# Optimization experiments

Measured on AMD Instinct MI355X. Metric: run time of the kernel, lower is better.

The kernel has to match this reference:

```python
import jax, jax.numpy as jnp
import numpy as np

B, S, E, H = 8, 2048, 1024, 64

def setup_inputs() -> dict:
    key = jax.random.key(0)
    k1, k2, k3, k4 = jax.random.split(key, 4)
    scale = 0.02
    return {
        "x": jax.random.normal(k1, (B, S, E), dtype=jnp.float32),
        "Wq": jax.random.normal(k2, (E, H), dtype=jnp.float32) * scale,
        "Wk": jax.random.normal(k3, (E, H), dtype=jnp.float32) * scale,
        "Wv": jax.random.normal(k4, (E, H), dtype=jnp.float32) * scale,
    }

def reference(x, Wq, Wk, Wv):
    # x: [B, S, E]; projections to [B, S, H]
    q = jnp.einsum("bse,eh->bsh", x, Wq)
    k = jnp.einsum("bse,eh->bsh", x, Wk)
    v = jnp.einsum("bse,eh->bsh", x, Wv)
    head_size = Wq.shape[1]
    # NOTE: original divides by head_size (not sqrt(head_size))
    scores = jnp.einsum("bqh,bkh->bqk", q, k) / head_size  # [B, S, S]
    seq = q.shape[1]
    causal = jnp.tril(jnp.ones((seq, seq), dtype=bool))
    scores = jnp.where(causal, scores, -jnp.inf)
    attn = jax.nn.softmax(scores, axis=-1)
    # dropout p=0.0 (eval) -> identity
    return jnp.einsum("bqk,bkh->bqh", attn, v)
```

## Files before the change

kernel.cpp:

```cpp
#include <hip/hip_runtime.h>


typedef __bf16 bf16;
typedef bf16 bf16x8 __attribute__((ext_vector_type(8)));
typedef bf16 bf16x4 __attribute__((ext_vector_type(4)));
typedef float v4f __attribute__((ext_vector_type(4)));

#define MFMA_BF16 __builtin_amdgcn_mfma_f32_16x16x32_bf16

constexpr int SEQ = 2048, EDIM = 1024, HDIM = 64;
constexpr float SCALE_L2E = 1.4426950408889634f / 64.0f;

#define AS1 __attribute__((address_space(1)))
#define AS3 __attribute__((address_space(3)))
static __device__ __forceinline__ void gload_lds16(const void* g, void* l) {
  __builtin_amdgcn_global_load_lds((const AS1 unsigned int*)g,
                                   (AS3 unsigned int*)l, 16, 0, 0);
}

__global__ __launch_bounds__(256) void prep_w_kernel(
    const float* __restrict__ Wq, const float* __restrict__ Wk,
    const float* __restrict__ Wv, bf16* __restrict__ Wt) {
  int mat = blockIdx.x >> 5, kseg = blockIdx.x & 31;
  const float* src = mat == 0 ? Wq : (mat == 1 ? Wk : Wv);
  int n = threadIdx.x & 63;
  int k0 = kseg * 32 + (threadIdx.x >> 6) * 8;
  bf16x8 v;
#pragma unroll
  for (int j = 0; j < 8; ++j)
    v[j] = (bf16)src[(k0 + j) * 64 + n];
  *reinterpret_cast<bf16x8*>(Wt + (size_t)(mat * 64 + n) * EDIM + k0) = v;
}

__global__ __launch_bounds__(256, 3) void proj_kernel(
    const float* __restrict__ x, const bf16* __restrict__ Wt,
    bf16* __restrict__ qw, bf16* __restrict__ kw, bf16* __restrict__ vT) {
  __shared__ __align__(16) bf16 Bs[2][192][64];
  __shared__ __align__(16) bf16 Ash[32][64];

  const int t = threadIdx.x;
  const int m0 = blockIdx.x * 32;
  const int wv = t >> 6, lane = t & 63, quad = lane >> 4, l16 = lane & 15;
  const int arow = t >> 3;
  const int aslot = t & 7;

  v4f acc[2][3] = {};
  float4 aR0, aR1;

  auto loadA = [&](int kk) {
    const float* p = x + (size_t)(m0 + arow) * EDIM + kk * 64 + aslot * 8;
    aR0 = *reinterpret_cast<const float4*>(p);
    aR1 = *reinterpret_cast<const float4*>(p + 4);
  };
  auto writeA = [&]() {
    bf16x8 h = {(bf16)aR0.x, (bf16)aR0.y, (bf16)aR0.z, (bf16)aR0.w,
                (bf16)aR1.x, (bf16)aR1.y, (bf16)aR1.z, (bf16)aR1.w};
    *reinterpret_cast<bf16x8*>((char*)&Ash[0][0] + arow * 128 +
                               ((aslot ^ (arow & 7)) * 16)) = h;
  };
  auto issueB = [&](int kk, int buf) {
#pragma unroll
    for (int p = 0; p < 6; ++p) {
      int q = p * 64 + lane;
      int r = 48 * wv + (q >> 3), s = q & 7;
      const bf16* src = Wt + (size_t)r * EDIM + kk * 64 + (s ^ (r & 7)) * 8;
      bf16* dst = &Bs[buf][48 * wv + 8 * p][0];
      gload_lds16(src, dst);
    }
  };

  loadA(0);
  issueB(0, 0);
  asm volatile("s_waitcnt vmcnt(6)" ::: "memory");
  __builtin_amdgcn_sched_barrier(0);
  writeA();
  asm volatile("s_waitcnt lgkmcnt(0)" ::: "memory");
  __builtin_amdgcn_s_barrier();

#pragma unroll 1
  for (int kk = 0; kk < 16; ++kk) {
    const int buf = kk & 1;
    if (kk < 15) {
      loadA(kk + 1);
      issueB(kk + 1, buf ^ 1);
      asm volatile("s_waitcnt vmcnt(8)" ::: "memory");
    } else {
      asm volatile("s_waitcnt vmcnt(0)" ::: "memory");
    }
    __builtin_amdgcn_sched_barrier(0);

    const char* asb = (const char*)&Ash[0][0];
    const char* bsb = (const char*)&Bs[buf][0][0];
    bf16x8 af[2][2];
#pragma unroll
    for (int mi = 0; mi < 2; ++mi)
#pragma unroll
      for (int ks = 0; ks < 2; ++ks) {
        int row = 16 * mi + l16;
        int off = ((4 * ks + quad) ^ (row & 7)) * 16;
        af[mi][ks] = *reinterpret_cast<const bf16x8*>(asb + row * 128 + off);
      }
#pragma unroll
    for (int ks = 0; ks < 2; ++ks) {
      bf16x8 bfr[3];
#pragma unroll
      for (int ni = 0; ni < 3; ++ni) {
        int R = 48 * wv + 16 * ni + l16;
        int off = (ks * 64 + quad * 16) ^ ((R & 7) << 4);
        bfr[ni] = *reinterpret_cast<const bf16x8*>(bsb + R * 128 + off);
      }
#pragma unroll
      for (int mi = 0; mi < 2; ++mi)
#pragma unroll
        for (int ni = 0; ni < 3; ++ni)
          acc[mi][ni] = MFMA_BF16(af[mi][ks], bfr[ni], acc[mi][ni], 0, 0, 0);
    }

    if (kk < 15) {
      asm volatile("s_waitcnt lgkmcnt(0)" ::: "memory");
      __builtin_amdgcn_sched_barrier(0);
      __builtin_amdgcn_s_barrier();
      asm volatile("s_waitcnt vmcnt(6)" ::: "memory");
      __builtin_amdgcn_sched_barrier(0);
      writeA();
      asm volatile("s_waitcnt lgkmcnt(0)" ::: "memory");
      __builtin_amdgcn_sched_barrier(0);
      __builtin_amdgcn_s_barrier();
    }
  }

#pragma unroll
  for (int mi = 0; mi < 2; ++mi) {
    const int token0 = m0 + 16 * mi + 4 * quad;
#pragma unroll
    for (int ni = 0; ni < 3; ++ni) {
      int n = 48 * wv + 16 * ni + l16;
      if (n < 64) {
#pragma unroll
        for (int r = 0; r < 4; ++r)
          qw[(size_t)(token0 + r) * HDIM + n] = (bf16)acc[mi][ni][r];
      } else if (n < 128) {
#pragma unroll
        for (int r = 0; r < 4; ++r)
          kw[(size_t)(token0 + r) * HDIM + (n - 64)] = (bf16)acc[mi][ni][r];
      } else {
        int b = token0 >> 11, s0 = token0 & 2047;
        bf16x4 pk = {(bf16)acc[mi][ni][0], (bf16)acc[mi][ni][1],
                     (bf16)acc[mi][ni][2], (bf16)acc[mi][ni][3]};
        *reinterpret_cast<bf16x4*>(
            vT + ((size_t)(b * 64 + (n - 128))) * SEQ + s0) = pk;
      }
    }
  }
}

__global__ __launch_bounds__(512) void attn_kernel(
    const bf16* __restrict__ qw, const bf16* __restrict__ kw,
    const bf16* __restrict__ vT, float* __restrict__ out) {
  const int batch = blockIdx.x & 7;
  const int pi = blockIdx.x >> 3;
  const int w = threadIdx.x >> 6;
  const int lane = threadIdx.x & 63;
  const int quad = lane >> 4, l16 = lane & 15;

  __shared__ __align__(16) bf16 p_lds[8][2][32][68];
  __shared__ __align__(16) float o_lds[8][32][68];
  __shared__ float l_lds[8][32];

  const bf16* qB = qw + (size_t)batch * SEQ * HDIM;
  const bf16* kB = kw + (size_t)batch * SEQ * HDIM;
  const bf16* vB = vT + (size_t)batch * HDIM * SEQ;

  for (int sp = 0; sp < 2; ++sp) {
    const int j = sp ? (63 - pi) : pi;
    const int q0 = 32 * j;
    const int T64 = (j + 2) >> 1;
    const int nw = (T64 > w) ? (((T64 - 1 - w) >> 3) + 1) : 0;

    bf16x8 aq[2][2];
#pragma unroll
    for (int mi = 0; mi < 2; ++mi)
#pragma unroll
      for (int kf = 0; kf < 2; ++kf)
        aq[mi][kf] = *reinterpret_cast<const bf16x8*>(
            qB + (size_t)(q0 + 16 * mi + l16) * HDIM + 32 * kf + 8 * quad);

    v4f accO[2][4] = {};
    float l_part[2][4] = {{0.f, 0.f, 0.f, 0.f}, {0.f, 0.f, 0.f, 0.f}};
    bf16x8 kfr[4][2];

    auto loadK = [&](int jt) {
#pragma unroll
      for (int nt = 0; nt < 4; ++nt)
#pragma unroll
        for (int kf = 0; kf < 2; ++kf)
          kfr[nt][kf] = *reinterpret_cast<const bf16x8*>(
              kB + (size_t)(64 * jt + 16 * nt + l16) * HDIM + 32 * kf +
              8 * quad);
    };
    auto qk_exp_stage = [&](int jt, int slot) {
      v4f s[2][4] = {};
#pragma unroll
      for (int mi = 0; mi < 2; ++mi)
#pragma unroll
        for (int nt = 0; nt < 4; ++nt) {
          s[mi][nt] = MFMA_BF16(aq[mi][0], kfr[nt][0], s[mi][nt], 0, 0, 0);
          s[mi][nt] = MFMA_BF16(aq[mi][1], kfr[nt][1], s[mi][nt], 0, 0, 0);
        }
      const bool last = (jt == T64 - 1);
#pragma unroll
      for (int mi = 0; mi < 2; ++mi)
#pragma unroll
        for (int nt = 0; nt < 4; ++nt)
#pragma unroll
          for (int r = 0; r < 4; ++r) {
            float p = __builtin_amdgcn_exp2f(s[mi][nt][r] * SCALE_L2E);
            if (last &&
                (64 * jt + 16 * nt + l16 > q0 + 16 * mi + 4 * quad + r))
              p = 0.f;
            l_part[mi][r] += p;
            p_lds[w][slot][16 * mi + 4 * quad + r][16 * nt + l16] = (bf16)p;
          }
    };

    if (nw > 0) {
      loadK(w);
      qk_exp_stage(w, 0);
    }
    for (int i = 0; i < nw; ++i) {
      const int jt = w + 8 * i;
      const int k0 = 64 * jt;
      if (i + 1 < nw) loadK(jt + 8);
      bf16x8 vfr[4][2];
#pragma unroll
      for (int nt = 0; nt < 4; ++nt)
#pragma unroll
        for (int kc = 0; kc < 2; ++kc)
          vfr[nt][kc] = *reinterpret_cast<const bf16x8*>(
              vB + (size_t)(16 * nt + l16) * SEQ + k0 + 32 * kc + 8 * quad);
      asm volatile("s_waitcnt lgkmcnt(0)" ::: "memory");
      bf16x8 pa[2][2];
#pragma unroll
      for (int mi = 0; mi < 2; ++mi)
#pragma unroll
        for (int kc = 0; kc < 2; ++kc)
          pa[mi][kc] = *reinterpret_cast<const bf16x8*>(
              &p_lds[w][i & 1][16 * mi + l16][32 * kc + 8 * quad]);
      if (i + 1 < nw) qk_exp_stage(jt + 8, (i + 1) & 1);
#pragma unroll
      for (int mi = 0; mi < 2; ++mi)
#pragma unroll
        for (int nt = 0; nt < 4; ++nt) {
          accO[mi][nt] = MFMA_BF16(pa[mi][0], vfr[nt][0], accO[mi][nt], 0, 0, 0);
          accO[mi][nt] = MFMA_BF16(pa[mi][1], vfr[nt][1], accO[mi][nt], 0, 0, 0);
        }
    }

#pragma unroll
    for (int mi = 0; mi < 2; ++mi)
#pragma unroll
      for (int r = 0; r < 4; ++r) {
        float s = l_part[mi][r];
        s += __shfl_xor(s, 1, 16);
        s += __shfl_xor(s, 2, 16);
        s += __shfl_xor(s, 4, 16);
        s += __shfl_xor(s, 8, 16);
        l_part[mi][r] = s;
      }

    __syncthreads();
#pragma unroll
    for (int mi = 0; mi < 2; ++mi)
#pragma unroll
      for (int nt = 0; nt < 4; ++nt)
#pragma unroll
        for (int r = 0; r < 4; ++r)
          o_lds[w][16 * mi + 4 * quad + r][16 * nt + l16] = accO[mi][nt][r];
    if (l16 == 0) {
#pragma unroll
      for (int mi = 0; mi < 2; ++mi)
#pragma unroll
        for (int r = 0; r < 4; ++r)
          l_lds[w][16 * mi + 4 * quad + r] = l_part[mi][r];
    }
    __syncthreads();

    {
      const int col = threadIdx.x & 63;
      const int r0 = (threadIdx.x >> 6) * 4;
#pragma unroll
      for (int k = 0; k < 4; ++k) {
        const int row = r0 + k;
        float lt = 0.f, s = 0.f;
#pragma unroll
        for (int c = 0; c < 8; ++c) {
          lt += l_lds[c][row];
          s += o_lds[c][row][col];
        }
        out[((size_t)batch * SEQ + q0 + row) * HDIM + col] = s / lt;
      }
    }
  }
}

extern "C" void kernel_launch(void* const* d_in, const int* in_sizes, int n_in,
                              void* d_out, int out_size, void* d_ws,
                              size_t ws_size, hipStream_t stream) {
  const float* x = (const float*)d_in[0];
  const float* Wq = (const float*)d_in[1];
  const float* Wk = (const float*)d_in[2];
  const float* Wv = (const float*)d_in[3];

  char* ws = (char*)d_ws;
  bf16* Wt = (bf16*)(ws);
  bf16* qw = (bf16*)(ws + 0x60000);
  bf16* kw = (bf16*)(ws + 0x260000);
  bf16* vT = (bf16*)(ws + 0x460000);

  prep_w_kernel<<<96, 256, 0, stream>>>(Wq, Wk, Wv, Wt);
  proj_kernel<<<512, 256, 0, stream>>>(x, Wt, qw, kw, vT);
  attn_kernel<<<256, 512, 0, stream>>>(qw, kw, vT, (float*)d_out);
}
```

Measured before the change: 138.3 us.

## Alias attention LDS buffers and split paired query tiles into separate blocks

Overlays the P staging buffer and the O reduction buffer in one shared allocation, halving LDS use per block so two blocks can be resident per CU. The grid doubles and each block now handles a single query tile instead of a balanced pair of short and long tiles. A launch-bounds occupancy hint is added. This trades the per-block causal load balancing for higher occupancy and latency hiding, and risks register pressure from the tighter bound.

```diff
diff --git a/kernel.cpp b/kernel.cpp
--- a/kernel.cpp
+++ b/kernel.cpp
@@ -154,151 +154,152 @@
   }
 }
 
-__global__ __launch_bounds__(512) void attn_kernel(
+__global__ __launch_bounds__(512, 4) void attn_kernel(
     const bf16* __restrict__ qw, const bf16* __restrict__ kw,
     const bf16* __restrict__ vT, float* __restrict__ out) {
-  const int batch = blockIdx.x & 7;
-  const int pi = blockIdx.x >> 3;
+  const int bid = blockIdx.x;
+  const int batch = bid & 7;
+  const int s = (bid & 255) >> 3;
+  const int j = (bid >= 256) ? (63 - s) : s;
   const int w = threadIdx.x >> 6;
   const int lane = threadIdx.x & 63;
   const int quad = lane >> 4, l16 = lane & 15;
 
-  __shared__ __align__(16) bf16 p_lds[8][2][32][68];
-  __shared__ __align__(16) float o_lds[8][32][68];
-  __shared__ float l_lds[8][32];
+  __shared__ __align__(16) char smem[70656];
+  typedef bf16 PT[2][32][68];
+  typedef float OT[32][68];
+  PT* p_lds = reinterpret_cast<PT*>(smem);
+  OT* o_lds = reinterpret_cast<OT*>(smem);
+  float(*l_lds)[32] = reinterpret_cast<float(*)[32]>(smem + 69632);
 
   const bf16* qB = qw + (size_t)batch * SEQ * HDIM;
   const bf16* kB = kw + (size_t)batch * SEQ * HDIM;
   const bf16* vB = vT + (size_t)batch * HDIM * SEQ;
 
-  for (int sp = 0; sp < 2; ++sp) {
-    const int j = sp ? (63 - pi) : pi;
-    const int q0 = 32 * j;
-    const int T64 = (j + 2) >> 1;
-    const int nw = (T64 > w) ? (((T64 - 1 - w) >> 3) + 1) : 0;
-
-    bf16x8 aq[2][2];
-#pragma unroll
-    for (int mi = 0; mi < 2; ++mi)
+  const int q0 = 32 * j;
+  const int T64 = (j + 2) >> 1;
+  const int nw = (T64 > w) ? (((T64 - 1 - w) >> 3) + 1) : 0;
+
+  bf16x8 aq[2][2];
+#pragma unroll
+  for (int mi = 0; mi < 2; ++mi)
+#pragma unroll
+    for (int kf = 0; kf < 2; ++kf)
+      aq[mi][kf] = *reinterpret_cast<const bf16x8*>(
+          qB + (size_t)(q0 + 16 * mi + l16) * HDIM + 32 * kf + 8 * quad);
+
+  v4f accO[2][4] = {};
+  float l_part[2][4] = {{0.f, 0.f, 0.f, 0.f}, {0.f, 0.f, 0.f, 0.f}};
+  bf16x8 kfr[4][2];
+
+  auto loadK = [&](int jt) {
+#pragma unroll
+    for (int nt = 0; nt < 4; ++nt)
 #pragma unroll
       for (int kf = 0; kf < 2; ++kf)
-        aq[mi][kf] = *reinterpret_cast<const bf16x8*>(
-            qB + (size_t)(q0 + 16 * mi + l16) * HDIM + 32 * kf + 8 * quad);
-
-    v4f accO[2][4] = {};
-    float l_part[2][4] = {{0.f, 0.f, 0.f, 0.f}, {0.f, 0.f, 0.f, 0.f}};
-    bf16x8 kfr[4][2];
-
-    auto loadK = [&](int jt) {
+        kfr[nt][kf] = *reinterpret_cast<const bf16x8*>(
+            kB + (size_t)(64 * jt + 16 * nt + l16) * HDIM + 32 * kf +
+            8 * quad);
+  };
+  auto qk_exp_stage = [&](int jt, int slot) {
+    v4f sc[2][4] = {};
+#pragma unroll
+    for (int mi = 0; mi < 2; ++mi)
+#pragma unroll
+      for (int nt = 0; nt < 4; ++nt) {
+        sc[mi][nt] = MFMA_BF16(aq[mi][0], kfr[nt][0], sc[mi][nt], 0, 0, 0);
+        sc[mi][nt] = MFMA_BF16(aq[mi][1], kfr[nt][1], sc[mi][nt], 0, 0, 0);
+      }
+    const bool last = (jt == T64 - 1);
+#pragma unroll
+    for (int mi = 0; mi < 2; ++mi)
 #pragma unroll
       for (int nt = 0; nt < 4; ++nt)
 #pragma unroll
-        for (int kf = 0; kf < 2; ++kf)
-          kfr[nt][kf] = *reinterpret_cast<const bf16x8*>(
-              kB + (size_t)(64 * jt + 16 * nt + l16) * HDIM + 32 * kf +
-              8 * quad);
-    };
-    auto qk_exp_stage = [&](int jt, int slot) {
-      v4f s[2][4] = {};
-#pragma unroll
-      for (int mi = 0; mi < 2; ++mi)
-#pragma unroll
-        for (int nt = 0; nt < 4; ++nt) {
-          s[mi][nt] = MFMA_BF16(aq[mi][0], kfr[nt][0], s[mi][nt], 0, 0, 0);
-          s[mi][nt] = MFMA_BF16(aq[mi][1], kfr[nt][1], s[mi][nt], 0, 0, 0);
+        for (int r = 0; r < 4; ++r) {
+          float p = __builtin_amdgcn_exp2f(sc[mi][nt][r] * SCALE_L2E);
+          if (last && (64 * jt + 16 * nt + l16 > q0 + 16 * mi + 4 * quad + r))
+            p = 0.f;
+          l_part[mi][r] += p;
+          p_lds[w][slot][16 * mi + 4 * quad + r][16 * nt + l16] = (bf16)p;
         }
-      const bool last = (jt == T64 - 1);
-#pragma unroll
-      for (int mi = 0; mi < 2; ++mi)
-#pragma unroll
-        for (int nt = 0; nt < 4; ++nt)
-#pragma unroll
-          for (int r = 0; r < 4; ++r) {
-            float p = __builtin_amdgcn_exp2f(s[mi][nt][r] * SCALE_L2E);
-            if (last &&
-                (64 * jt + 16 * nt + l16 > q0 + 16 * mi + 4 * quad + r))
-              p = 0.f;
-            l_part[mi][r] += p;
-            p_lds[w][slot][16 * mi + 4 * quad + r][16 * nt + l16] = (bf16)p;
-          }
-    };
-
-    if (nw > 0) {
-      loadK(w);
-      qk_exp_stage(w, 0);
-    }
-    for (int i = 0; i < nw; ++i) {
-      const int jt = w + 8 * i;
-      const int k0 = 64 * jt;
-      if (i + 1 < nw) loadK(jt + 8);
-      bf16x8 vfr[4][2];
-#pragma unroll
-      for (int nt = 0; nt < 4; ++nt)
-#pragma unroll
-        for (int kc = 0; kc < 2; ++kc)
-          vfr[nt][kc] = *reinterpret_cast<const bf16x8*>(
-              vB + (size_t)(16 * nt + l16) * SEQ + k0 + 32 * kc + 8 * quad);
-      asm volatile("s_waitcnt lgkmcnt(0)" ::: "memory");
-      bf16x8 pa[2][2];
-#pragma unroll
-      for (int mi = 0; mi < 2; ++mi)
-#pragma unroll
-        for (int kc = 0; kc < 2; ++kc)
-          pa[mi][kc] = *reinterpret_cast<const bf16x8*>(
-              &p_lds[w][i & 1][16 * mi + l16][32 * kc + 8 * quad]);
-      if (i + 1 < nw) qk_exp_stage(jt + 8, (i + 1) & 1);
-#pragma unroll
-      for (int mi = 0; mi < 2; ++mi)
-#pragma unroll
-        for (int nt = 0; nt < 4; ++nt) {
-          accO[mi][nt] = MFMA_BF16(pa[mi][0], vfr[nt][0], accO[mi][nt], 0, 0, 0);
-          accO[mi][nt] = MFMA_BF16(pa[mi][1], vfr[nt][1], accO[mi][nt], 0, 0, 0);
-        }
-    }
-
-#pragma unroll
-    for (int mi = 0; mi < 2; ++mi)
-#pragma unroll
-      for (int r = 0; r < 4; ++r) {
-        float s = l_part[mi][r];
-        s += __shfl_xor(s, 1, 16);
-        s += __shfl_xor(s, 2, 16);
-        s += __shfl_xor(s, 4, 16);
-        s += __shfl_xor(s, 8, 16);
-        l_part[mi][r] = s;
-      }
-
-    __syncthreads();
-#pragma unroll
-    for (int mi = 0; mi < 2; ++mi)
-#pragma unroll
-      for (int nt = 0; nt < 4; ++nt)
-#pragma unroll
-        for (int r = 0; r < 4; ++r)
-          o_lds[w][16 * mi + 4 * quad + r][16 * nt + l16] = accO[mi][nt][r];
-    if (l16 == 0) {
-#pragma unroll
-      for (int mi = 0; mi < 2; ++mi)
-#pragma unroll
-        for (int r = 0; r < 4; ++r)
-          l_lds[w][16 * mi + 4 * quad + r] = l_part[mi][r];
-    }
-    __syncthreads();
-
-    {
-      const int col = threadIdx.x & 63;
-      const int r0 = (threadIdx.x >> 6) * 4;
-#pragma unroll
-      for (int k = 0; k < 4; ++k) {
-        const int row = r0 + k;
-        float lt = 0.f, s = 0.f;
-#pragma unroll
-        for (int c = 0; c < 8; ++c) {
-          lt += l_lds[c][row];
-          s += o_lds[c][row][col];
-        }
-        out[((size_t)batch * SEQ + q0 + row) * HDIM + col] = s / lt;
-      }
+  };
+
+  if (nw > 0) {
+    loadK(w);
+    qk_exp_stage(w, 0);
+  }
+  for (int i = 0; i < nw; ++i) {
+    const int jt = w + 8 * i;
+    const int k0 = 64 * jt;
+    if (i + 1 < nw) loadK(jt + 8);
+    bf16x8 vfr[4][2];
+#pragma unroll
+    for (int nt = 0; nt < 4; ++nt)
+#pragma unroll
+      for (int kc = 0; kc < 2; ++kc)
+        vfr[nt][kc] = *reinterpret_cast<const bf16x8*>(
+            vB + (size_t)(16 * nt + l16) * SEQ + k0 + 32 * kc + 8 * quad);
+    asm volatile("s_waitcnt lgkmcnt(0)" ::: "memory");
+    bf16x8 pa[2][2];
+#pragma unroll
+    for (int mi = 0; mi < 2; ++mi)
+#pragma unroll
+      for (int kc = 0; kc < 2; ++kc)
+        pa[mi][kc] = *reinterpret_cast<const bf16x8*>(
+            &p_lds[w][i & 1][16 * mi + l16][32 * kc + 8 * quad]);
+    if (i + 1 < nw) qk_exp_stage(jt + 8, (i + 1) & 1);
+#pragma unroll
+    for (int mi = 0; mi < 2; ++mi)
+#pragma unroll
+      for (int nt = 0; nt < 4; ++nt) {
+        accO[mi][nt] = MFMA_BF16(pa[mi][0], vfr[nt][0], accO[mi][nt], 0, 0, 0);
+        accO[mi][nt] = MFMA_BF16(pa[mi][1], vfr[nt][1], accO[mi][nt], 0, 0, 0);
+      }
+  }
+
+#pragma unroll
+  for (int mi = 0; mi < 2; ++mi)
+#pragma unroll
+    for (int r = 0; r < 4; ++r) {
+      float sv = l_part[mi][r];
+      sv += __shfl_xor(sv, 1, 16);
+      sv += __shfl_xor(sv, 2, 16);
+      sv += __shfl_xor(sv, 4, 16);
+      sv += __shfl_xor(sv, 8, 16);
+      l_part[mi][r] = sv;
+    }
+
+  __syncthreads();
+#pragma unroll
+  for (int mi = 0; mi < 2; ++mi)
+#pragma unroll
+    for (int nt = 0; nt < 4; ++nt)
+#pragma unroll
+      for (int r = 0; r < 4; ++r)
+        o_lds[w][16 * mi + 4 * quad + r][16 * nt + l16] = accO[mi][nt][r];
+  if (l16 == 0) {
+#pragma unroll
+    for (int mi = 0; mi < 2; ++mi)
+#pragma unroll
+      for (int r = 0; r < 4; ++r)
+        l_lds[w][16 * mi + 4 * quad + r] = l_part[mi][r];
+  }
+  __syncthreads();
+
+  {
+    const int col = threadIdx.x & 63;
+    const int r0 = (threadIdx.x >> 6) * 4;
+#pragma unroll
+    for (int k = 0; k < 4; ++k) {
+      const int row = r0 + k;
+      float lt = 0.f, sv = 0.f;
+#pragma unroll
+      for (int c = 0; c < 8; ++c) {
+        lt += l_lds[c][row];
+        sv += o_lds[c][row][col];
+      }
+      out[((size_t)batch * SEQ + q0 + row) * HDIM + col] = sv / lt;
     }
   }
 }
@@ -319,5 +320,5 @@
 
   prep_w_kernel<<<96, 256, 0, stream>>>(Wq, Wk, Wv, Wt);
   proj_kernel<<<512, 256, 0, stream>>>(x, Wt, qw, kw, vT);
-  attn_kernel<<<256, 512, 0, stream>>>(qw, kw, vT, (float*)d_out);
-}
+  attn_kernel<<<512, 512, 0, stream>>>(qw, kw, vT, (float*)d_out);
+}
```

Measured after the change: 180.2 us. 30.3% more time.
